# Kernel tuning notes

Measured on AMD Instinct MI355X. Metric: run time of the kernel, lower is better.

## Reference

```python
import jax, jax.numpy as jnp
import numpy as np

B, S, F, H, W = 16, 2048, 512, 512, 5
PAD = W // 2


def setup_inputs() -> dict:
    key = jax.random.key(0)
    k = jax.random.split(key, 6)
    scale = 0.02
    return {
        "embeds_output": jax.random.normal(k[0], (B, S, F), dtype=jnp.float32),
        "Wq": jax.random.normal(k[1], (F, H), dtype=jnp.float32) * scale,
        "Wk": jax.random.normal(k[2], (F, H), dtype=jnp.float32) * scale,
        "v_att": jax.random.normal(k[3], (H,), dtype=jnp.float32) * scale,
        "cnn_W": jax.random.normal(k[4], (W * F, H), dtype=jnp.float32) * scale,
        "cnn_b": jax.random.normal(k[5], (H,), dtype=jnp.float32) * scale,
    }


def reference(embeds_output, Wq, Wk, v_att, cnn_W, cnn_b):
    b, s, f = embeds_output.shape
    # getConvEmbeds: zero-pad and gather W shifted views -> [B, S, W, F]
    xp = jnp.pad(embeds_output, ((0, 0), (PAD, PAD), (0, 0)))
    windows = jnp.stack([xp[:, i:i + s, :] for i in range(W)], axis=2)  # [B,S,W,F]
    entity = windows[:, :, PAD, :]  # center token, [B,S,F]
    # Bahdanau additive attention over the window
    q = jnp.einsum('bsf,fh->bsh', entity, Wq)          # [B,S,H]
    kproj = jnp.einsum('bswf,fh->bswh', windows, Wk)   # [B,S,W,H]
    scores = jnp.einsum('bswh,h->bsw', jnp.tanh(kproj + q[:, :, None, :]), v_att)
    att = jax.nn.softmax(scores, axis=-1)              # [B,S,W]
    # weight contexts, flatten window dim (row-major W*F, matching torch reshape)
    att_context = (att[..., None] * windows).reshape(b, s, W * F)
    return att_context @ cnn_W + cnn_b                 # [B,S,H]
```

## Files before the change

kernel.cpp:

```cpp
#include <hip/hip_runtime.h>
#include <stdint.h>
#include <stddef.h>

typedef unsigned short u16;
typedef __attribute__((ext_vector_type(8))) short s16x8;
typedef __attribute__((ext_vector_type(8))) unsigned short u16x8;
typedef __attribute__((ext_vector_type(4))) unsigned short u16x4;
typedef __attribute__((ext_vector_type(4))) float f32x4;

typedef __attribute__((address_space(3))) void* as3_void_p;
typedef const __attribute__((address_space(1))) void* as1_cvoid_p;

#define GLD16(gp, lp) __builtin_amdgcn_global_load_lds((as1_cvoid_p)(gp), (as3_void_p)(lp), 16, 0, 0)

enum {
  NS = 2048, NF = 512, NH = 512, NW = 5,
  NROW = 32768,
  K2 = NW * NF
};

__device__ __forceinline__ u16 f2bf(float f) {
  unsigned u = __float_as_uint(f);
  u += 0x7FFFu + ((u >> 16) & 1u);
  return (u16)(u >> 16);
}
__device__ __forceinline__ float bf2f(u16 v) {
  return __uint_as_float(((unsigned)v) << 16);
}


__global__ __launch_bounds__(256) void cvtX(const float* __restrict__ X, u16* __restrict__ Xb) {
  int i = blockIdx.x * 256 + threadIdx.x;
  f32x4 v = ((const f32x4*)X)[i];
  u16x4 o;
  o.x = f2bf(v.x); o.y = f2bf(v.y); o.z = f2bf(v.z); o.w = f2bf(v.w);
  ((u16x4*)Xb)[i] = o;
}

__global__ __launch_bounds__(256) void cvtW(const float* __restrict__ Wq, const float* __restrict__ Wk,
                                            const float* __restrict__ cnnW,
                                            u16* __restrict__ Wt1, u16* __restrict__ Wt2) {
  int i = blockIdx.x * 256 + threadIdx.x;
  if (i < 1024 * 512) {
    int j = i >> 9, f = i & 511;
    float v = (j < 512) ? Wq[(size_t)f * 512 + j] : Wk[(size_t)f * 512 + (j - 512)];
    Wt1[i] = f2bf(v);
  } else {
    int t = i - 1024 * 512;
    int h = t / K2, k = t % K2;
    Wt2[t] = f2bf(cnnW[(size_t)k * 512 + h]);
  }
}


__global__ __launch_bounds__(256) void gemm_qk(const u16* __restrict__ Xb,
                                               const u16* __restrict__ Wt1,
                                               u16* __restrict__ QKb) {
  __shared__ u16 As[128 * 64];
  __shared__ u16 Bs[128 * 64];
  const int tid  = threadIdx.x;
  const int lane = tid & 63, wid = tid >> 6;
  const int wr = wid >> 1, wc = wid & 1;
  const int fr = lane & 15, fq = lane >> 4;
  const int wgid = (blockIdx.x & 7) * 256 + (blockIdx.x >> 3);
  const int brow = (wgid >> 3) * 128;
  const int bcol = (wgid & 7) * 128;

  f32x4 acc[4][4] = {};

  for (int kt = 0; kt < 8; ++kt) {
#pragma unroll
    for (int p = 0; p < 4; ++p) {
      int off = (p * 256 + tid) * 16;
      int r = off >> 7;
      int cb = (off & 127) ^ ((r & 7) << 4);
      const u16* ga = Xb  + (size_t)(brow + r) * NF + kt * 64 + (cb >> 1);
      const u16* gb = Wt1 + (size_t)(bcol + r) * NF + kt * 64 + (cb >> 1);
      GLD16(ga, (char*)As + off);
      GLD16(gb, (char*)Bs + off);
    }
    __syncthreads();
#pragma unroll
    for (int kk = 0; kk < 2; ++kk) {
      s16x8 af[4], bfr[4];
#pragma unroll
      for (int m = 0; m < 4; ++m) {
        int row = wr * 64 + m * 16 + fr;
        af[m] = *(const s16x8*)((const char*)As + row * 128 + ((kk * 64 + fq * 16) ^ ((row & 7) << 4)));
      }
#pragma unroll
      for (int n = 0; n < 4; ++n) {
        int row = wc * 64 + n * 16 + fr;
        bfr[n] = *(const s16x8*)((const char*)Bs + row * 128 + ((kk * 64 + fq * 16) ^ ((row & 7) << 4)));
      }
#pragma unroll
      for (int m = 0; m < 4; ++m)
#pragma unroll
        for (int n = 0; n < 4; ++n)
          acc[m][n] = __builtin_amdgcn_mfma_f32_16x16x32_bf16(af[m], bfr[n], acc[m][n], 0, 0, 0);
    }
    __syncthreads();
  }

#pragma unroll
  for (int m = 0; m < 4; ++m)
#pragma unroll
    for (int n = 0; n < 4; ++n)
#pragma unroll
      for (int r = 0; r < 4; ++r) {
        int row = brow + wr * 64 + m * 16 + fq * 4 + r;
        int col = bcol + wc * 64 + n * 16 + fr;
        QKb[(size_t)row * 1024 + col] = f2bf(acc[m][n][r]);
      }
}


__global__ __launch_bounds__(256) void scores_att(const u16* __restrict__ QKb,
                                                  const float* __restrict__ vatt,
                                                  float* __restrict__ att) {
  const int lane = threadIdx.x & 63;
  const int wid  = threadIdx.x >> 6;
  const int n = blockIdx.x * 4 + wid;
  const int s = n & (NS - 1);
  const int h0 = lane * 8;

  u16x8 qv = *(const u16x8*)(QKb + (size_t)n * 1024 + h0);
  f32x4 va0 = *(const f32x4*)(vatt + h0);
  f32x4 va1 = *(const f32x4*)(vatt + h0 + 4);
  float q[8], vv[8];
#pragma unroll
  for (int j = 0; j < 8; ++j) q[j] = bf2f(qv[j]);
  vv[0] = va0.x; vv[1] = va0.y; vv[2] = va0.z; vv[3] = va0.w;
  vv[4] = va1.x; vv[5] = va1.y; vv[6] = va1.z; vv[7] = va1.w;

  float sc[5];
#pragma unroll
  for (int w = 0; w < 5; ++w) {
    int sp = s + w - 2;
    u16x8 kv = {0, 0, 0, 0, 0, 0, 0, 0};
    if (sp >= 0 && sp < NS)
      kv = *(const u16x8*)(QKb + (size_t)(n + w - 2) * 1024 + 512 + h0);
    float acc = 0.f;
#pragma unroll
    for (int j = 0; j < 8; ++j) {
      float x = q[j] + bf2f(kv[j]);
      x = fminf(fmaxf(x, -15.f), 15.f);
      float e = __expf(2.f * x);
      acc += vv[j] * ((e - 1.f) / (e + 1.f));
    }
    sc[w] = acc;
  }
#pragma unroll
  for (int w = 0; w < 5; ++w)
#pragma unroll
    for (int o = 32; o > 0; o >>= 1)
      sc[w] += __shfl_xor(sc[w], o, 64);

  if (lane == 0) {
    float m = sc[0];
#pragma unroll
    for (int w = 1; w < 5; ++w) m = fmaxf(m, sc[w]);
    float e[5], sum = 0.f;
#pragma unroll
    for (int w = 0; w < 5; ++w) { e[w] = __expf(sc[w] - m); sum += e[w]; }
    float inv = 1.f / sum;
#pragma unroll
    for (int w = 0; w < 5; ++w) att[(size_t)n * 5 + w] = e[w] * inv;
  }
}


__global__ __launch_bounds__(512, 4) void gemm_out(const u16* __restrict__ Xb,
                                                   const u16* __restrict__ Wt2,
                                                   const float* __restrict__ att,
                                                   const float* __restrict__ cnnb,
                                                   float* __restrict__ out) {
  __shared__ u16 As[128 * 64];
  __shared__ u16 Bs[128 * 64];
  __shared__ float att_s[128 * 5];
  const int tid  = threadIdx.x;
  const int lane = tid & 63, wid = tid >> 6;
  const int wr = wid >> 2, wc = wid & 3;
  const int fr = lane & 15, fq = lane >> 4;
  const int wgid = (blockIdx.x & 7) * 128 + (blockIdx.x >> 3);
  const int brow = (wgid >> 2) * 128;
  const int bcol = (wgid & 3) * 128;

  if (tid < 128) {
    int s = (brow + tid) & (NS - 1);
#pragma unroll
    for (int w = 0; w < 5; ++w) {
      int sp = s + w - 2;
      att_s[tid * 5 + w] = (sp >= 0 && sp < NS) ? att[(size_t)(brow + tid) * 5 + w] : 0.f;
    }
  }

  const int rsub = tid >> 3;
  const int cb   = (((tid & 7) ^ (rsub & 7)) << 4);
  const int ldsA0 = tid * 16;
  const int ldsA1 = 8192 + tid * 16;
  const int ldsB0 = tid * 16;
  const int ldsB1 = 8192 + tid * 16;
  const char* gB0 = (const char*)(Wt2 + (size_t)(bcol + rsub) * K2) + cb;
  const char* gB1 = (const char*)(Wt2 + (size_t)(bcol + 64 + rsub) * K2) + cb;

  f32x4 acc[4][2] = {};
  f32x4 accOut[4][2] = {};

  for (int w = 0; w < 5; ++w) {
    int g0 = brow + rsub + w - 2;
    int g1 = brow + 64 + rsub + w - 2;
    g0 = g0 < 0 ? 0 : (g0 >= NROW ? NROW - 1 : g0);
    g1 = g1 < 0 ? 0 : (g1 >= NROW ? NROW - 1 : g1);
    const char* gA0 = (const char*)(Xb + (size_t)g0 * NF) + cb;
    const char* gA1 = (const char*)(Xb + (size_t)g1 * NF) + cb;
    const char* gBw0 = gB0 + w * 1024;
    const char* gBw1 = gB1 + w * 1024;

    for (int kt = 0; kt < 8; ++kt) {
      GLD16(gA0  + kt * 128, (char*)As + ldsA0);
      GLD16(gA1  + kt * 128, (char*)As + ldsA1);
      GLD16(gBw0 + kt * 128, (char*)Bs + ldsB0);
      GLD16(gBw1 + kt * 128, (char*)Bs + ldsB1);
      __syncthreads();
#pragma unroll
      for (int kk = 0; kk < 2; ++kk) {
        s16x8 af[4], bfr[2];
#pragma unroll
        for (int m = 0; m < 4; ++m) {
          int row = wr * 64 + m * 16 + fr;
          af[m] = *(const s16x8*)((const char*)As + row * 128 + ((kk * 64 + fq * 16) ^ ((row & 7) << 4)));
        }
#pragma unroll
        for (int n = 0; n < 2; ++n) {
          int row = wc * 32 + n * 16 + fr;
          bfr[n] = *(const s16x8*)((const char*)Bs + row * 128 + ((kk * 64 + fq * 16) ^ ((row & 7) << 4)));
        }
#pragma unroll
        for (int m = 0; m < 4; ++m)
#pragma unroll
          for (int n = 0; n < 2; ++n)
            acc[m][n] = __builtin_amdgcn_mfma_f32_16x16x32_bf16(af[m], bfr[n], acc[m][n], 0, 0, 0);
      }
      __syncthreads();
    }
#pragma unroll
    for (int m = 0; m < 4; ++m) {
      float a0 = att_s[(wr * 64 + m * 16 + fq * 4 + 0) * 5 + w];
      float a1 = att_s[(wr * 64 + m * 16 + fq * 4 + 1) * 5 + w];
      float a2 = att_s[(wr * 64 + m * 16 + fq * 4 + 2) * 5 + w];
      float a3 = att_s[(wr * 64 + m * 16 + fq * 4 + 3) * 5 + w];
#pragma unroll
      for (int n = 0; n < 2; ++n) {
        accOut[m][n][0] += a0 * acc[m][n][0];
        accOut[m][n][1] += a1 * acc[m][n][1];
        accOut[m][n][2] += a2 * acc[m][n][2];
        accOut[m][n][3] += a3 * acc[m][n][3];
        acc[m][n] = f32x4{0.f, 0.f, 0.f, 0.f};
      }
    }
  }

#pragma unroll
  for (int m = 0; m < 4; ++m)
#pragma unroll
    for (int n = 0; n < 2; ++n)
#pragma unroll
      for (int r = 0; r < 4; ++r) {
        int row = brow + wr * 64 + m * 16 + fq * 4 + r;
        int col = bcol + wc * 32 + n * 16 + fr;
        out[(size_t)row * NH + col] = accOut[m][n][r] + cnnb[col];
      }
}


extern "C" void kernel_launch(void* const* d_in, const int* in_sizes, int n_in,
                              void* d_out, int out_size, void* d_ws, size_t ws_size,
                              hipStream_t stream) {
  const float* X    = (const float*)d_in[0];
  const float* Wq   = (const float*)d_in[1];
  const float* Wk   = (const float*)d_in[2];
  const float* vatt = (const float*)d_in[3];
  const float* cnnW = (const float*)d_in[4];
  const float* cnnb = (const float*)d_in[5];
  float* out = (float*)d_out;

  char* ws = (char*)d_ws;
  u16*   Xb  = (u16*)ws;
  u16*   Wt1 = (u16*)(ws + 33554432);
  u16*   Wt2 = (u16*)(ws + 34603008);
  u16*   QKb = (u16*)(ws + 37224448);
  float* att = (float*)(ws + 104333312);

  cvtX<<<dim3(NROW * NF / 4 / 256), dim3(256), 0, stream>>>(X, Xb);
  cvtW<<<dim3((1024 * 512 + 512 * K2) / 256), dim3(256), 0, stream>>>(Wq, Wk, cnnW, Wt1, Wt2);
  gemm_qk<<<dim3(2048), dim3(256), 0, stream>>>(Xb, Wt1, QKb);
  scores_att<<<dim3(NROW / 4), dim3(256), 0, stream>>>(QKb, vatt, att);
  gemm_out<<<dim3(1024), dim3(512), 0, stream>>>(Xb, Wt2, att, cnnb, out);
}
```

Before: 208.7 us.

## Double-buffer LDS tiles in both GEMMs and widen gemm_qk to 512 threads

Both GEMM kernels now keep two LDS buffers and issue the global-to-LDS loads for the next K-tile before computing on the current one. This overlaps memory latency with the MFMA work and needs only one barrier per iteration. gemm_out flattens its window and K loops into a single 40-step pipeline so prefetching continues across window boundaries. gemm_qk moves to 512 threads with 8 waves, each computing a 64x32 sub-tile, which matches gemm_out's layout. The cost is double the LDS footprint per block, which may reduce occupancy.

```diff
diff --git a/kernel.cpp b/kernel.cpp
--- a/kernel.cpp
+++ b/kernel.cpp
@@ -53,63 +53,76 @@
 }
 
 
-__global__ __launch_bounds__(256) void gemm_qk(const u16* __restrict__ Xb,
-                                               const u16* __restrict__ Wt1,
-                                               u16* __restrict__ QKb) {
-  __shared__ u16 As[128 * 64];
-  __shared__ u16 Bs[128 * 64];
+__global__ __launch_bounds__(512, 4) void gemm_qk(const u16* __restrict__ Xb,
+                                                  const u16* __restrict__ Wt1,
+                                                  u16* __restrict__ QKb) {
+  __shared__ u16 As[2][128 * 64];
+  __shared__ u16 Bs[2][128 * 64];
   const int tid  = threadIdx.x;
   const int lane = tid & 63, wid = tid >> 6;
-  const int wr = wid >> 1, wc = wid & 1;
+  const int wr = wid >> 2, wc = wid & 3;
   const int fr = lane & 15, fq = lane >> 4;
   const int wgid = (blockIdx.x & 7) * 256 + (blockIdx.x >> 3);
   const int brow = (wgid >> 3) * 128;
   const int bcol = (wgid & 7) * 128;
 
-  f32x4 acc[4][4] = {};
-
+  const int rsub = tid >> 3;
+  const int cb   = (((tid & 7) ^ (rsub & 7)) << 4);
+  const char* gA0 = (const char*)(Xb  + (size_t)(brow + rsub) * NF) + cb;
+  const char* gA1 = (const char*)(Xb  + (size_t)(brow + 64 + rsub) * NF) + cb;
+  const char* gB0 = (const char*)(Wt1 + (size_t)(bcol + rsub) * NF) + cb;
+  const char* gB1 = (const char*)(Wt1 + (size_t)(bcol + 64 + rsub) * NF) + cb;
+
+  f32x4 acc[4][2] = {};
+
+  GLD16(gA0, (char*)As[0] + tid * 16);
+  GLD16(gA1, (char*)As[0] + 8192 + tid * 16);
+  GLD16(gB0, (char*)Bs[0] + tid * 16);
+  GLD16(gB1, (char*)Bs[0] + 8192 + tid * 16);
+  __syncthreads();
+
+  int cur = 0;
   for (int kt = 0; kt < 8; ++kt) {
-#pragma unroll
-    for (int p = 0; p < 4; ++p) {
-      int off = (p * 256 + tid) * 16;
-      int r = off >> 7;
-      int cb = (off & 127) ^ ((r & 7) << 4);
-      const u16* ga = Xb  + (size_t)(brow + r) * NF + kt * 64 + (cb >> 1);
-      const u16* gb = Wt1 + (size_t)(bcol + r) * NF + kt * 64 + (cb >> 1);
-      GLD16(ga, (char*)As + off);
-      GLD16(gb, (char*)Bs + off);
-    }
-    __syncthreads();
+    if (kt + 1 < 8) {
+      int o = (kt + 1) * 128;
+      GLD16(gA0 + o, (char*)As[cur ^ 1] + tid * 16);
+      GLD16(gA1 + o, (char*)As[cur ^ 1] + 8192 + tid * 16);
+      GLD16(gB0 + o, (char*)Bs[cur ^ 1] + tid * 16);
+      GLD16(gB1 + o, (char*)Bs[cur ^ 1] + 8192 + tid * 16);
+    }
+    const char* Ab = (const char*)As[cur];
+    const char* Bb = (const char*)Bs[cur];
 #pragma unroll
     for (int kk = 0; kk < 2; ++kk) {
-      s16x8 af[4], bfr[4];
+      s16x8 af[4], bfr[2];
 #pragma unroll
       for (int m = 0; m < 4; ++m) {
         int row = wr * 64 + m * 16 + fr;
-        af[m] = *(const s16x8*)((const char*)As + row * 128 + ((kk * 64 + fq * 16) ^ ((row & 7) << 4)));
-      }
-#pragma unroll
-      for (int n = 0; n < 4; ++n) {
-        int row = wc * 64 + n * 16 + fr;
-        bfr[n] = *(const s16x8*)((const char*)Bs + row * 128 + ((kk * 64 + fq * 16) ^ ((row & 7) << 4)));
+        af[m] = *(const s16x8*)(Ab + row * 128 + ((kk * 64 + fq * 16) ^ ((row & 7) << 4)));
+      }
+#pragma unroll
+      for (int n = 0; n < 2; ++n) {
+        int row = wc * 32 + n * 16 + fr;
+        bfr[n] = *(const s16x8*)(Bb + row * 128 + ((kk * 64 + fq * 16) ^ ((row & 7) << 4)));
       }
 #pragma unroll
       for (int m = 0; m < 4; ++m)
 #pragma unroll
-        for (int n = 0; n < 4; ++n)
+        for (int n = 0; n < 2; ++n)
           acc[m][n] = __builtin_amdgcn_mfma_f32_16x16x32_bf16(af[m], bfr[n], acc[m][n], 0, 0, 0);
     }
     __syncthreads();
+    cur ^= 1;
   }
 
 #pragma unroll
   for (int m = 0; m < 4; ++m)
 #pragma unroll
-    for (int n = 0; n < 4; ++n)
+    for (int n = 0; n < 2; ++n)
 #pragma unroll
       for (int r = 0; r < 4; ++r) {
         int row = brow + wr * 64 + m * 16 + fq * 4 + r;
-        int col = bcol + wc * 64 + n * 16 + fr;
+        int col = bcol + wc * 32 + n * 16 + fr;
         QKb[(size_t)row * 1024 + col] = f2bf(acc[m][n][r]);
       }
 }
@@ -175,8 +188,8 @@
                                                    const float* __restrict__ att,
                                                    const float* __restrict__ cnnb,
                                                    float* __restrict__ out) {
-  __shared__ u16 As[128 * 64];
-  __shared__ u16 Bs[128 * 64];
+  __shared__ u16 As[2][128 * 64];
+  __shared__ u16 Bs[2][128 * 64];
   __shared__ float att_s[128 * 5];
   const int tid  = threadIdx.x;
   const int lane = tid & 63, wid = tid >> 6;
@@ -197,68 +210,72 @@
 
   const int rsub = tid >> 3;
   const int cb   = (((tid & 7) ^ (rsub & 7)) << 4);
-  const int ldsA0 = tid * 16;
-  const int ldsA1 = 8192 + tid * 16;
-  const int ldsB0 = tid * 16;
-  const int ldsB1 = 8192 + tid * 16;
   const char* gB0 = (const char*)(Wt2 + (size_t)(bcol + rsub) * K2) + cb;
   const char* gB1 = (const char*)(Wt2 + (size_t)(bcol + 64 + rsub) * K2) + cb;
 
+  auto stage = [&](int buf, int it) {
+    int wn = it >> 3, ktn = it & 7;
+    int g0 = brow + rsub + wn - 2;
+    int g1 = brow + 64 + rsub + wn - 2;
+    g0 = g0 < 0 ? 0 : (g0 >= NROW ? NROW - 1 : g0);
+    g1 = g1 < 0 ? 0 : (g1 >= NROW ? NROW - 1 : g1);
+    int ko = ktn * 128;
+    GLD16((const char*)(Xb + (size_t)g0 * NF) + cb + ko, (char*)As[buf] + tid * 16);
+    GLD16((const char*)(Xb + (size_t)g1 * NF) + cb + ko, (char*)As[buf] + 8192 + tid * 16);
+    GLD16(gB0 + wn * 1024 + ko, (char*)Bs[buf] + tid * 16);
+    GLD16(gB1 + wn * 1024 + ko, (char*)Bs[buf] + 8192 + tid * 16);
+  };
+
   f32x4 acc[4][2] = {};
   f32x4 accOut[4][2] = {};
 
-  for (int w = 0; w < 5; ++w) {
-    int g0 = brow + rsub + w - 2;
-    int g1 = brow + 64 + rsub + w - 2;
-    g0 = g0 < 0 ? 0 : (g0 >= NROW ? NROW - 1 : g0);
-    g1 = g1 < 0 ? 0 : (g1 >= NROW ? NROW - 1 : g1);
-    const char* gA0 = (const char*)(Xb + (size_t)g0 * NF) + cb;
-    const char* gA1 = (const char*)(Xb + (size_t)g1 * NF) + cb;
-    const char* gBw0 = gB0 + w * 1024;
-    const char* gBw1 = gB1 + w * 1024;
-
-    for (int kt = 0; kt < 8; ++kt) {
-      GLD16(gA0  + kt * 128, (char*)As + ldsA0);
-      GLD16(gA1  + kt * 128, (char*)As + ldsA1);
-      GLD16(gBw0 + kt * 128, (char*)Bs + ldsB0);
-      GLD16(gBw1 + kt * 128, (char*)Bs + ldsB1);
-      __syncthreads();
-#pragma unroll
-      for (int kk = 0; kk < 2; ++kk) {
-        s16x8 af[4], bfr[2];
-#pragma unroll
-        for (int m = 0; m < 4; ++m) {
-          int row = wr * 64 + m * 16 + fr;
-          af[m] = *(const s16x8*)((const char*)As + row * 128 + ((kk * 64 + fq * 16) ^ ((row & 7) << 4)));
+  stage(0, 0);
+  __syncthreads();
+
+  int cur = 0;
+  for (int it = 0; it < 40; ++it) {
+    if (it + 1 < 40) stage(cur ^ 1, it + 1);
+    const char* Ab = (const char*)As[cur];
+    const char* Bb = (const char*)Bs[cur];
+#pragma unroll
+    for (int kk = 0; kk < 2; ++kk) {
+      s16x8 af[4], bfr[2];
+#pragma unroll
+      for (int m = 0; m < 4; ++m) {
+        int row = wr * 64 + m * 16 + fr;
+        af[m] = *(const s16x8*)(Ab + row * 128 + ((kk * 64 + fq * 16) ^ ((row & 7) << 4)));
+      }
+#pragma unroll
+      for (int n = 0; n < 2; ++n) {
+        int row = wc * 32 + n * 16 + fr;
+        bfr[n] = *(const s16x8*)(Bb + row * 128 + ((kk * 64 + fq * 16) ^ ((row & 7) << 4)));
+      }
+#pragma unroll
+      for (int m = 0; m < 4; ++m)
+#pragma unroll
+        for (int n = 0; n < 2; ++n)
+          acc[m][n] = __builtin_amdgcn_mfma_f32_16x16x32_bf16(af[m], bfr[n], acc[m][n], 0, 0, 0);
+    }
+    if ((it & 7) == 7) {
+      int w = it >> 3;
+#pragma unroll
+      for (int m = 0; m < 4; ++m) {
+        float a0 = att_s[(wr * 64 + m * 16 + fq * 4 + 0) * 5 + w];
+        float a1 = att_s[(wr * 64 + m * 16 + fq * 4 + 1) * 5 + w];
+        float a2 = att_s[(wr * 64 + m * 16 + fq * 4 + 2) * 5 + w];
+        float a3 = att_s[(wr * 64 + m * 16 + fq * 4 + 3) * 5 + w];
+#pragma unroll
+        for (int n = 0; n < 2; ++n) {
+          accOut[m][n][0] += a0 * acc[m][n][0];
+          accOut[m][n][1] += a1 * acc[m][n][1];
+          accOut[m][n][2] += a2 * acc[m][n][2];
+          accOut[m][n][3] += a3 * acc[m][n][3];
+          acc[m][n] = f32x4{0.f, 0.f, 0.f, 0.f};
         }
-#pragma unroll
-        for (int n = 0; n < 2; ++n) {
-          int row = wc * 32 + n * 16 + fr;
-          bfr[n] = *(const s16x8*)((const char*)Bs + row * 128 + ((kk * 64 + fq * 16) ^ ((row & 7) << 4)));
-        }
-#pragma unroll
-        for (int m = 0; m < 4; ++m)
-#pragma unroll
-          for (int n = 0; n < 2; ++n)
-            acc[m][n] = __builtin_amdgcn_mfma_f32_16x16x32_bf16(af[m], bfr[n], acc[m][n], 0, 0, 0);
-      }
-      __syncthreads();
-    }
-#pragma unroll
-    for (int m = 0; m < 4; ++m) {
-      float a0 = att_s[(wr * 64 + m * 16 + fq * 4 + 0) * 5 + w];
-      float a1 = att_s[(wr * 64 + m * 16 + fq * 4 + 1) * 5 + w];
-      float a2 = att_s[(wr * 64 + m * 16 + fq * 4 + 2) * 5 + w];
-      float a3 = att_s[(wr * 64 + m * 16 + fq * 4 + 3) * 5 + w];
-#pragma unroll
-      for (int n = 0; n < 2; ++n) {
-        accOut[m][n][0] += a0 * acc[m][n][0];
-        accOut[m][n][1] += a1 * acc[m][n][1];
-        accOut[m][n][2] += a2 * acc[m][n][2];
-        accOut[m][n][3] += a3 * acc[m][n][3];
-        acc[m][n] = f32x4{0.f, 0.f, 0.f, 0.f};
-      }
-    }
+      }
+    }
+    __syncthreads();
+    cur ^= 1;
   }
 
 #pragma unroll
@@ -294,7 +311,7 @@
 
   cvtX<<<dim3(NROW * NF / 4 / 256), dim3(256), 0, stream>>>(X, Xb);
   cvtW<<<dim3((1024 * 512 + 512 * K2) / 256), dim3(256), 0, stream>>>(Wq, Wk, cnnW, Wt1, Wt2);
-  gemm_qk<<<dim3(2048), dim3(256), 0, stream>>>(Xb, Wt1, QKb);
+  gemm_qk<<<dim3(2048), dim3(512), 0, stream>>>(Xb, Wt1, QKb);
   scores_att<<<dim3(NROW / 4), dim3(256), 0, stream>>>(QKb, vatt, att);
   gemm_out<<<dim3(1024), dim3(512), 0, stream>>>(Xb, Wt2, att, cnnb, out);
 }
```

After: 215.2 us. 1.03x slower.
